# Optimization experiments

Measured on AMD Instinct MI355X. Metric: run time of the kernel, lower is better.

Reference implementation:

```python
import jax, jax.numpy as jnp
import numpy as np

VOCAB, EMB, QLEN, DLEN, K = 100000, 300, 256, 8192, 5


def prelu(x, a):
    return jnp.where(x >= 0, x, a * x)


def apply_conv(x, filt, a):
    # x: (L, E), filt: (E, 1, fs, E) -- matches torch F.conv2d(OIHW)
    fs = filt.shape[2]
    pad = fs // 2 + 1
    inp = x[None, None, :, :]  # (1,1,L,E)
    out = jax.lax.conv_general_dilated(
        inp, filt, window_strides=(1, 1), padding=[(pad, pad), (0, 0)],
        dimension_numbers=('NCHW', 'OIHW', 'NCHW'))  # (1,E,L',1)
    out = prelu(out, a)
    out = out[:, :, -x.shape[0]:, 0]          # keep last L rows -> (1,E,L)
    out = jnp.transpose(out, (0, 2, 1))[0]    # (L,E)
    return out + x


def cosine_sim(A, B):
    # (Q,E) x (D,E) -> (Q,D)
    num = A @ B.T
    den = jnp.linalg.norm(A, axis=1)[:, None] * jnp.linalg.norm(B, axis=1)[None, :]
    return num / den


def pool(sim):
    # sort-based k-max pooling == top_k (same set of values)
    top = jax.lax.top_k(sim, K)[0]           # (Q,K) descending
    avg = top.sum(-1) / float(K)
    mx = top[..., 0]
    return jnp.stack([mx, avg], axis=-1)      # (Q,2)


def score(pooled_list, w1, b1, w2, b2, a1, a2):
    x = jnp.concatenate(pooled_list, axis=-1)  # (Q,8)
    lo = prelu(x @ w1.T + b1, a1)              # dropout is identity in eval
    lo = prelu(lo @ w2.T + b2, a2)[..., 0]     # (Q,)
    return lo.sum(-1) / lo.shape[-1]


def setup_inputs() -> dict:
    key = jax.random.key(0)
    ks = jax.random.split(key, 12)
    doc1 = jax.random.randint(ks[0], (DLEN,), 0, VOCAB)
    doc2 = jax.random.randint(ks[1], (DLEN,), 0, VOCAB)
    question = jax.random.randint(ks[2], (QLEN,), 0, VOCAB)
    doc1_sim = jax.random.uniform(ks[3], (DLEN, QLEN), dtype=jnp.float32)
    doc2_sim = jax.random.uniform(ks[4], (DLEN, QLEN), dtype=jnp.float32)
    embeds = jax.random.normal(ks[5], (VOCAB, EMB), dtype=jnp.float32)
    filt_bi = jax.random.normal(ks[6], (EMB, 1, 2, EMB), dtype=jnp.float32)
    filt_tri = jax.random.normal(ks[7], (EMB, 1, 3, EMB), dtype=jnp.float32)
    w1 = jax.random.normal(ks[8], (8, 8), dtype=jnp.float32) * 0.3
    b1 = jnp.zeros((8,), jnp.float32)
    w2 = jax.random.normal(ks[9], (1, 8), dtype=jnp.float32) * 0.3
    b2 = jnp.zeros((1,), jnp.float32)
    a_bi = jnp.float32(0.25); a_tri = jnp.float32(0.25)
    a1 = jnp.float32(0.25); a2 = jnp.float32(0.25)
    return dict(doc1=doc1, doc2=doc2, question=question, doc1_sim=doc1_sim,
                doc2_sim=doc2_sim, embeds=embeds, filt_bi=filt_bi,
                filt_tri=filt_tri, a_bi=a_bi, a_tri=a_tri, w1=w1, b1=b1,
                w2=w2, b2=b2, a1=a1, a2=a2)


def reference(doc1, doc2, question, doc1_sim, doc2_sim, embeds, filt_bi,
              filt_tri, a_bi, a_tri, w1, b1, w2, b2, a1, a2):
    sim_oh1 = doc1_sim.T  # (Q,D)
    sim_oh2 = doc2_sim.T
    qe = embeds[question]
    d1e = embeds[doc1]
    d2e = embeds[doc2]
    qmask = (question > 1).astype(jnp.float32)
    m1 = qmask[:, None] * (doc1 > 1).astype(jnp.float32)[None, :]
    m2 = qmask[:, None] * (doc2 > 1).astype(jnp.float32)[None, :]
    ins1 = cosine_sim(qe, d1e) * m1
    ins2 = cosine_sim(qe, d2e) * m2
    q_bi = apply_conv(qe, filt_bi, a_bi)
    q_tri = apply_conv(qe, filt_tri, a_tri)
    d1_bi = apply_conv(d1e, filt_bi, a_bi)
    d1_tri = apply_conv(d1e, filt_tri, a_tri)
    d2_bi = apply_conv(d2e, filt_bi, a_bi)
    d2_tri = apply_conv(d2e, filt_tri, a_tri)
    s1_bi = cosine_sim(q_bi, d1_bi)
    s2_bi = cosine_sim(q_bi, d2_bi)
    s1_tri = cosine_sim(q_tri, d1_tri)
    s2_tri = cosine_sim(q_tri, d2_tri)
    d1_emit = score([pool(sim_oh1), pool(ins1), pool(s1_bi), pool(s1_tri)],
                    w1, b1, w2, b2, a1, a2)
    d2_emit = score([pool(sim_oh2), pool(ins2), pool(s2_bi), pool(s2_tri)],
                    w1, b1, w2, b2, a1, a2)
    # MarginRankingLoss(margin=0.9), y=1, batch of 1
    loss1 = jnp.maximum(0.0, -(d1_emit - d2_emit) + 0.9)
    loss2 = loss1 * 0.0
    return (loss1, d1_emit, d2_emit, loss1, loss2)
```

## Files before the change

### kernel.cpp

```cpp
#include <hip/hip_runtime.h>

#define EMB   300
#define QLEN  256
#define DLEN  8192
#define KTOP  5
#define STR   320
#define STRB  640

typedef __attribute__((ext_vector_type(8))) short short8v;
typedef __attribute__((ext_vector_type(4))) float f32x4;

__device__ inline float bf2f(short u) {
    return __uint_as_float(((unsigned int)(unsigned short)u) << 16);
}
__device__ inline short f2bf(float f) {
    unsigned int x = __float_as_uint(f);
    unsigned int r = x + 0x7fffu + ((x >> 16) & 1u);
    return (short)(r >> 16);
}
__device__ inline void gload_lds16(const void* g, void* l) {
    __builtin_amdgcn_global_load_lds((const __attribute__((address_space(1))) void*)g,
                                     (__attribute__((address_space(3))) void*)l, 16, 0, 0);
}
__device__ inline int swz128(int a) { return a ^ (((a >> 7) & 7) << 4); }

#define INSERT5(arr, v)                                                          \
    if ((v) > arr[4]) {                                                          \
        arr[4] = (v);                                                            \
        if (arr[4] > arr[3]) { float t_ = arr[4]; arr[4] = arr[3]; arr[3] = t_; }\
        if (arr[3] > arr[2]) { float t_ = arr[3]; arr[3] = arr[2]; arr[2] = t_; }\
        if (arr[2] > arr[1]) { float t_ = arr[2]; arr[2] = arr[1]; arr[1] = t_; }\
        if (arr[1] > arr[0]) { float t_ = arr[1]; arr[1] = arr[0]; arr[0] = t_; }\
    }

struct PrepArgs {
    const float* embeds;
    const int* toks[3]; short* out[3]; float* ssq[3]; int rows[3];
    const float* filt[2]; short* fout[2];
    float* convssq;
};

__global__ void prep(PrepArgs pa) {
    if (blockIdx.x >= 4646) {
        int idx = (blockIdx.x - 4646) * 256 + threadIdx.x;
        if (idx < 8320) {
            float4 z = {0.f, 0.f, 0.f, 0.f};
            *(float4*)(pa.convssq + idx * 4) = z;
        }
        return;
    }
    int W = blockIdx.x * 4 + (threadIdx.x >> 6);
    int lane = threadIdx.x & 63;
    int e0 = lane * 8;
    if (W < 16664) {
        int s, r;
        if (W < 264) { s = 0; r = W; }
        else if (W < 8464) { s = 1; r = W - 264; }
        else { s = 2; r = W - 8464; }
        int rows = pa.rows[s];
        short8v ov = {0, 0, 0, 0, 0, 0, 0, 0};
        float sum = 0.f;
        if (r < rows && e0 < 300) {
            const float* src = pa.embeds + (long)pa.toks[s][r] * EMB;
            float4 f0 = *(const float4*)(src + e0);
            ov[0] = f2bf(f0.x); ov[1] = f2bf(f0.y); ov[2] = f2bf(f0.z); ov[3] = f2bf(f0.w);
            sum = f0.x * f0.x + f0.y * f0.y + f0.z * f0.z + f0.w * f0.w;
            if (e0 < 296) {
                float4 f1 = *(const float4*)(src + e0 + 4);
                ov[4] = f2bf(f1.x); ov[5] = f2bf(f1.y); ov[6] = f2bf(f1.z); ov[7] = f2bf(f1.w);
                sum += f1.x * f1.x + f1.y * f1.y + f1.z * f1.z + f1.w * f1.w;
            }
        }
        if (e0 < STR) *(short8v*)(pa.out[s] + (long)r * STR + e0) = ov;
        #pragma unroll
        for (int off = 32; off > 0; off >>= 1) sum += __shfl_down(sum, off, 64);
        if (lane == 0 && r < rows) pa.ssq[s][r] = sum;
    } else {
        int w2 = W - 16664;
        int s = (w2 < 768) ? 0 : 1;
        int R = (s == 0) ? w2 : w2 - 768;
        int o = (s == 0) ? (R >> 1) : (R / 3);
        short8v ov = {0, 0, 0, 0, 0, 0, 0, 0};
        if (o < EMB && e0 < 300) {
            const float* src = pa.filt[s] + (long)R * EMB;
            float4 f0 = *(const float4*)(src + e0);
            ov[0] = f2bf(f0.x); ov[1] = f2bf(f0.y); ov[2] = f2bf(f0.z); ov[3] = f2bf(f0.w);
            if (e0 < 296) {
                float4 f1 = *(const float4*)(src + e0 + 4);
                ov[4] = f2bf(f1.x); ov[5] = f2bf(f1.y); ov[6] = f2bf(f1.z); ov[7] = f2bf(f1.w);
            }
        }
        if (e0 < STR) *(short8v*)(pa.fout[s] + (long)R * STR + e0) = ov;
    }
}

#define GEMM_PRELUDE64                                                        \
    int tid = threadIdx.x, lane = tid & 63, w = tid >> 6;                     \
    int wr = w >> 1, wc = w & 1;                                              \
    int arow[2], acol[2], brow[4], bcol[4];                                   \
    _Pragma("unroll")                                                         \
    for (int i_ = 0; i_ < 2; ++i_) {                                          \
        int lg_ = swz128(w * 2048 + i_ * 1024 + lane * 16);                   \
        arow[i_] = lg_ >> 7; acol[i_] = lg_ & 127;                            \
    }                                                                         \
    _Pragma("unroll")                                                         \
    for (int i_ = 0; i_ < 4; ++i_) {                                          \
        int lg_ = swz128(w * 4096 + i_ * 1024 + lane * 16);                   \
        brow[i_] = lg_ >> 7; bcol[i_] = lg_ & 127;                            \
    }

#define STAGE64(t) do { int kb_ = (t) * 128;                                  \
    _Pragma("unroll")                                                         \
    for (int i_ = 0; i_ < 2; ++i_)                                            \
        gload_lds16(Ab + (size_t)arow[i_] * STRB + kb_ + acol[i_],            \
                    AsB + w * 2048 + i_ * 1024);                              \
    _Pragma("unroll")                                                         \
    for (int i_ = 0; i_ < 4; ++i_)                                            \
        gload_lds16(Bb + (size_t)brow[i_] * ldbB + kb_ + bcol[i_],            \
                    BsB + w * 4096 + i_ * 1024);                              \
    } while (0)

#define COMPUTE64 do {                                                        \
    _Pragma("unroll")                                                         \
    for (int h_ = 0; h_ < 2; ++h_) {                                          \
        short8v a_[2], b_[4];                                                 \
        _Pragma("unroll")                                                     \
        for (int f_ = 0; f_ < 2; ++f_) {                                      \
            int la_ = (wr * 32 + f_ * 16 + (lane & 15)) * 128                 \
                      + ((lane >> 4) << 4) + h_ * 64;                         \
            a_[f_] = *(const short8v*)(AsB + swz128(la_));                    \
        }                                                                     \
        _Pragma("unroll")                                                     \
        for (int f_ = 0; f_ < 4; ++f_) {                                      \
            int lb_ = (wc * 64 + f_ * 16 + (lane & 15)) * 128                 \
                      + ((lane >> 4) << 4) + h_ * 64;                         \
            b_[f_] = *(const short8v*)(BsB + swz128(lb_));                    \
        }                                                                     \
        _Pragma("unroll")                                                     \
        for (int mf_ = 0; mf_ < 2; ++mf_)                                     \
            _Pragma("unroll")                                                 \
            for (int nf_ = 0; nf_ < 4; ++nf_)                                 \
                acc[mf_][nf_] = __builtin_amdgcn_mfma_f32_16x16x32_bf16(      \
                    a_[mf_], b_[nf_], acc[mf_][nf_], 0, 0, 0);                \
    } } while (0)

#define GEMM_MAIN64(nt) do {                                                  \
    for (int t_ = 0; t_ < (nt); ++t_) {                                       \
        if (t_ > 0) __syncthreads();                                          \
        STAGE64(t_);                                                          \
        __syncthreads();                                                      \
        COMPUTE64;                                                            \
    } } while (0)

__device__ inline void topk_reduce_store(float top[KTOP], float (*buf)[KTOP], int t,
                                         float* feat, int q, int c0) {
    #pragma unroll
    for (int i = 0; i < KTOP; ++i) buf[t][i] = top[i];
    __syncthreads();
    for (int stride = 128; stride >= 1; stride >>= 1) {
        if (t < stride) {
            float arr[KTOP];
            #pragma unroll
            for (int i = 0; i < KTOP; ++i) arr[i] = buf[t][i];
            #pragma unroll
            for (int r = 0; r < KTOP; ++r) { float v = buf[t + stride][r]; INSERT5(arr, v); }
            #pragma unroll
            for (int i = 0; i < KTOP; ++i) buf[t][i] = arr[i];
        }
        __syncthreads();
    }
    if (t == 0) {
        float mx = buf[0][0];
        float sum = buf[0][0] + buf[0][1] + buf[0][2] + buf[0][3] + buf[0][4];
        feat[(long)q * 8 + c0] = mx;
        feat[(long)q * 8 + c0 + 1] = sum / (float)KTOP;
    }
}

struct ConvSlice { const short* A; const short* F; short* O; float* ssq;
                   const float* alpha; int fs; int shift; };
struct ConvOhArgs { ConvSlice s[6]; const float* S1; const float* S2; float* part; };

__global__ __launch_bounds__(256) void conv_oh(ConvOhArgs args) {
    int orig = blockIdx.x;
    if (orig >= 1560) {
        int r2 = orig - 1560;
        int doc = r2 >> 7, dblk = r2 & 127;
        const float* S = doc == 0 ? args.S1 : args.S2;
        int t = threadIdx.x;
        const float* base = S + (size_t)dblk * 64 * QLEN + t;
        float top[KTOP];
        #pragma unroll
        for (int i = 0; i < KTOP; ++i) top[i] = -3.4e38f;
        float vb[16];
        #pragma unroll
        for (int g = 0; g < 4; ++g) {
            #pragma unroll
            for (int j = 0; j < 16; ++j)
                vb[j] = base[(size_t)(g * 16 + j) * QLEN];
            #pragma unroll
            for (int j = 0; j < 16; ++j) INSERT5(top, vb[j]);
        }
        float* dst = args.part + ((size_t)((6 + doc) * 128 + dblk) * QLEN + t) * KTOP;
        #pragma unroll
        for (int i = 0; i < KTOP; ++i) dst[i] = top[i];
        return;
    }
    int lin = orig;
    int o = (lin & 7) * 195 + (lin >> 3);
    int z;
    if (o < 384) { z = 3; }
    else if (o < 768) { z = 5; o -= 384; }
    else if (o < 780) { z = 1; o -= 768; }
    else if (o < 1164) { z = 2; o -= 780; }
    else if (o < 1548) { z = 4; o -= 1164; }
    else { z = 0; o -= 1548; }
    ConvSlice sl;
    switch (z) {
        case 0: sl = args.s[0]; break; case 1: sl = args.s[1]; break;
        case 2: sl = args.s[2]; break; case 3: sl = args.s[3]; break;
        case 4: sl = args.s[4]; break; default: sl = args.s[5]; break;
    }
    int x = o % 3, y = o / 3;
    int m0 = y * 64, n0 = x * 128;
    int ldbB = sl.fs * STRB;

    __shared__ char smem[24576];
    char* AsB = smem;
    char* BsB = smem + 8192;
    GEMM_PRELUDE64
    const char* Ab = (const char*)sl.A + (size_t)(m0 + sl.shift) * STRB;
    const char* Bb = (const char*)sl.F + (size_t)n0 * ldbB;
    int nt = sl.fs * 5;
    float al = *sl.alpha;

    f32x4 acc[2][4] = {};
    GEMM_MAIN64(nt);

    #pragma unroll
    for (int mf = 0; mf < 2; ++mf) {
        #pragma unroll
        for (int j = 0; j < 4; ++j) {
            int r = m0 + wr * 32 + mf * 16 + (lane >> 4) * 4 + j;
            float p = 0.f;
            #pragma unroll
            for (int nf = 0; nf < 4; ++nf) {
                int c = n0 + wc * 64 + nf * 16 + (lane & 15);
                short ov = 0;
                if (c < EMB) {
                    float v = acc[mf][nf][j];
                    v = v >= 0.f ? v : al * v;
                    v += bf2f(sl.A[(size_t)r * STR + c]);
                    ov = f2bf(v);
                    p += v * v;
                }
                if (c < STR) sl.O[(size_t)r * STR + c] = ov;
            }
            p += __shfl_xor(p, 1, 64);
            p += __shfl_xor(p, 2, 64);
            p += __shfl_xor(p, 4, 64);
            p += __shfl_xor(p, 8, 64);
            if ((lane & 15) == 0) atomicAdd(sl.ssq + r, p);
        }
    }
}

struct SimSlice { const short* D; const short* Q; const float* dssq; const float* qssq;
                  const int* dtok; int mask; };
struct SimArgs { SimSlice s[6]; const int* qtok; float* part; };

__global__ __launch_bounds__(256) void sim_mfma(SimArgs args) {
    int lin = blockIdx.x;
    int wk = (lin & 7) * 192 + (lin >> 3);
    int s = wk >> 8; int rem = wk & 255; int x = rem & 1; int dblk = rem >> 1;
    SimSlice sl;
    switch (s) {
        case 0: sl = args.s[0]; break; case 1: sl = args.s[1]; break;
        case 2: sl = args.s[2]; break; case 3: sl = args.s[3]; break;
        case 4: sl = args.s[4]; break; default: sl = args.s[5]; break;
    }
    int m0 = dblk * 64, n0 = x * 128;
    const int ldbB = STRB;

    __shared__ char AsB[8192];
    __shared__ char BsB[16384];
    GEMM_PRELUDE64
    const char* Ab = (const char*)sl.D + (size_t)m0 * STRB;
    const char* Bb = (const char*)sl.Q + (size_t)n0 * STRB;

    f32x4 acc[2][4] = {};
    GEMM_MAIN64(5);

    float dinvv[2][4];
    int dtokv[2][4];
    #pragma unroll
    for (int mf = 0; mf < 2; ++mf) {
        int r0 = m0 + wr * 32 + mf * 16 + (lane >> 4) * 4;
        float4 dv = *(const float4*)(sl.dssq + r0);
        dinvv[mf][0] = rsqrtf(dv.x); dinvv[mf][1] = rsqrtf(dv.y);
        dinvv[mf][2] = rsqrtf(dv.z); dinvv[mf][3] = rsqrtf(dv.w);
        if (sl.mask) {
            int4 tv = *(const int4*)(sl.dtok + r0);
            dtokv[mf][0] = tv.x; dtokv[mf][1] = tv.y; dtokv[mf][2] = tv.z; dtokv[mf][3] = tv.w;
        }
    }
    __syncthreads();
    float (*lds5)[128][KTOP] = (float (*)[128][KTOP])AsB;

    #pragma unroll
    for (int nf = 0; nf < 4; ++nf) {
        int c = n0 + wc * 64 + nf * 16 + (lane & 15);
        float qs = rsqrtf(sl.qssq[c]);
        bool qok = sl.mask ? (args.qtok[c] > 1) : true;
        float top[KTOP];
        #pragma unroll
        for (int i = 0; i < KTOP; ++i) top[i] = -3.4e38f;
        #pragma unroll
        for (int mf = 0; mf < 2; ++mf)
            #pragma unroll
            for (int j = 0; j < 4; ++j) {
                float v = acc[mf][nf][j] * qs * dinvv[mf][j];
                if (sl.mask && (!qok || dtokv[mf][j] <= 1)) v = 0.f;
                INSERT5(top, v);
            }
        #pragma unroll
        for (int st = 16; st <= 32; st <<= 1) {
            float o[KTOP];
            #pragma unroll
            for (int i = 0; i < KTOP; ++i) o[i] = __shfl_xor(top[i], st, 64);
            #pragma unroll
            for (int i = 0; i < KTOP; ++i) { float v = o[i]; INSERT5(top, v); }
        }
        if (lane < 16) {
            int ql = wc * 64 + nf * 16 + lane;
            #pragma unroll
            for (int i = 0; i < KTOP; ++i) lds5[wr][ql][i] = top[i];
        }
    }
    __syncthreads();
    if (tid < 128) {
        float arr[KTOP];
        #pragma unroll
        for (int i = 0; i < KTOP; ++i) arr[i] = lds5[0][tid][i];
        #pragma unroll
        for (int i = 0; i < KTOP; ++i) { float v = lds5[1][tid][i]; INSERT5(arr, v); }
        int q = n0 + tid;
        float* dst = args.part + ((size_t)(s * 128 + dblk) * QLEN + q) * KTOP;
        #pragma unroll
        for (int i = 0; i < KTOP; ++i) dst[i] = arr[i];
    }
}

__global__ void pool_reduce(const float* __restrict__ part,
                            float* __restrict__ feat1, float* __restrict__ feat2) {
    int s = blockIdx.y, q = blockIdx.x, t = threadIdx.x;
    __shared__ float buf[256][KTOP];
    float top[KTOP];
    #pragma unroll
    for (int i = 0; i < KTOP; ++i) top[i] = -3.4e38f;
    if (t < 128) {
        const float* src = part + ((size_t)(s * 128 + t) * QLEN + q) * KTOP;
        #pragma unroll
        for (int i = 0; i < KTOP; ++i) { float v = src[i]; INSERT5(top, v); }
    }
    float* feat = (s < 6) ? (s < 3 ? feat1 : feat2) : (s == 6 ? feat1 : feat2);
    int c0 = (s < 6) ? 2 + 2 * (s % 3) : 0;
    topk_reduce_store(top, buf, t, feat, q, c0);
}

__global__ void final_score(const float* __restrict__ feat1, const float* __restrict__ feat2,
                            const float* __restrict__ w1, const float* __restrict__ b1,
                            const float* __restrict__ w2, const float* __restrict__ b2,
                            const float* __restrict__ a1p, const float* __restrict__ a2p,
                            float* __restrict__ out) {
    __shared__ float s1buf[256], s2buf[256];
    int q = threadIdx.x;
    float a1 = *a1p, a2 = *a2p;
    float v[2];
    #pragma unroll
    for (int dsel = 0; dsel < 2; ++dsel) {
        const float* feat = dsel == 0 ? feat1 : feat2;
        float x[8];
        #pragma unroll
        for (int i = 0; i < 8; ++i) x[i] = feat[q * 8 + i];
        float lo[8];
        #pragma unroll
        for (int j = 0; j < 8; ++j) {
            float s = b1[j];
            #pragma unroll
            for (int i = 0; i < 8; ++i) s += x[i] * w1[j * 8 + i];
            lo[j] = s >= 0.f ? s : a1 * s;
        }
        float s2v = b2[0];
        #pragma unroll
        for (int j = 0; j < 8; ++j) s2v += lo[j] * w2[j];
        v[dsel] = s2v >= 0.f ? s2v : a2 * s2v;
    }
    s1buf[q] = v[0];
    s2buf[q] = v[1];
    __syncthreads();
    for (int st = 128; st >= 1; st >>= 1) {
        if (q < st) { s1buf[q] += s1buf[q + st]; s2buf[q] += s2buf[q + st]; }
        __syncthreads();
    }
    if (q == 0) {
        float d1 = s1buf[0] / (float)QLEN;
        float d2 = s2buf[0] / (float)QLEN;
        float loss1 = fmaxf(0.f, -(d1 - d2) + 0.9f);
        out[0] = loss1; out[1] = d1; out[2] = d2; out[3] = loss1; out[4] = 0.f;
    }
}

extern "C" void kernel_launch(void* const* d_in, const int* in_sizes, int n_in,
                              void* d_out, int out_size, void* d_ws, size_t ws_size,
                              hipStream_t stream) {
    const int*   doc1     = (const int*)d_in[0];
    const int*   doc2     = (const int*)d_in[1];
    const int*   question = (const int*)d_in[2];
    const float* doc1_sim = (const float*)d_in[3];
    const float* doc2_sim = (const float*)d_in[4];
    const float* embeds   = (const float*)d_in[5];
    const float* filt_bi  = (const float*)d_in[6];
    const float* filt_tri = (const float*)d_in[7];
    const float* a_bi     = (const float*)d_in[8];
    const float* a_tri    = (const float*)d_in[9];
    const float* w1       = (const float*)d_in[10];
    const float* b1       = (const float*)d_in[11];
    const float* w2       = (const float*)d_in[12];
    const float* b2       = (const float*)d_in[13];
    const float* a1       = (const float*)d_in[14];
    const float* a2       = (const float*)d_in[15];
    float* out = (float*)d_out;

    float* ws = (float*)d_ws;
    size_t off = 0;
    auto allocf = [&](size_t n) { float* p = ws + off; off += n; return p; };
    float* feat1 = allocf(QLEN * 8);
    float* feat2 = allocf(QLEN * 8);
    float* ssq_qe  = allocf(QLEN);
    float* ssq_d1e = allocf(DLEN);
    float* ssq_d2e = allocf(DLEN);
    float* convssq = allocf(2 * QLEN + 4 * DLEN);
    float* ssq_qbi  = convssq;
    float* ssq_qtri = convssq + QLEN;
    float* ssq_d1bi  = convssq + 2 * QLEN;
    float* ssq_d1tri = convssq + 2 * QLEN + DLEN;
    float* ssq_d2bi  = convssq + 2 * QLEN + 2 * DLEN;
    float* ssq_d2tri = convssq + 2 * QLEN + 3 * DLEN;
    float* part = allocf((size_t)8 * 128 * QLEN * KTOP);
    off = (off + 7) & ~(size_t)7;

    short* hb = (short*)(ws + off);
    size_t hoff = 0;
    auto alloch = [&](size_t n) { short* p = hb + hoff; hoff += n; return p; };
    const size_t QH = (size_t)(QLEN + 8) * STR;
    const size_t DH = (size_t)(DLEN + 8) * STR;
    short* qe_h   = alloch(QH);
    short* qbi_h  = alloch(QH);
    short* qtri_h = alloch(QH);
    short* d1e_h   = alloch(DH);
    short* d1bi_h  = alloch(DH);
    short* d1tri_h = alloch(DH);
    short* d2e_h   = alloch(DH);
    short* d2bi_h  = alloch(DH);
    short* d2tri_h = alloch(DH);
    short* fbi_h  = alloch((size_t)384 * 2 * STR);
    short* ftri_h = alloch((size_t)384 * 3 * STR);

    PrepArgs pa;
    pa.embeds = embeds;
    pa.toks[0] = question; pa.out[0] = qe_h;  pa.ssq[0] = ssq_qe;  pa.rows[0] = QLEN;
    pa.toks[1] = doc1;     pa.out[1] = d1e_h; pa.ssq[1] = ssq_d1e; pa.rows[1] = DLEN;
    pa.toks[2] = doc2;     pa.out[2] = d2e_h; pa.ssq[2] = ssq_d2e; pa.rows[2] = DLEN;
    pa.filt[0] = filt_bi;  pa.fout[0] = fbi_h;
    pa.filt[1] = filt_tri; pa.fout[1] = ftri_h;
    pa.convssq = convssq;
    prep<<<dim3(4679), 256, 0, stream>>>(pa);

    ConvOhArgs ca;
    ca.s[0] = { qe_h,  fbi_h,  qbi_h,  ssq_qbi,  a_bi,  2, 1 };
    ca.s[1] = { qe_h,  ftri_h, qtri_h, ssq_qtri, a_tri, 3, 0 };
    ca.s[2] = { d1e_h, fbi_h,  d1bi_h, ssq_d1bi, a_bi,  2, 1 };
    ca.s[3] = { d1e_h, ftri_h, d1tri_h,ssq_d1tri,a_tri, 3, 0 };
    ca.s[4] = { d2e_h, fbi_h,  d2bi_h, ssq_d2bi, a_bi,  2, 1 };
    ca.s[5] = { d2e_h, ftri_h, d2tri_h,ssq_d2tri,a_tri, 3, 0 };
    ca.S1 = doc1_sim; ca.S2 = doc2_sim;
    ca.part = part;
    conv_oh<<<dim3(1816), 256, 0, stream>>>(ca);

    SimArgs sa;
    sa.s[0] = { d1e_h,   qe_h,   ssq_d1e,   ssq_qe,   doc1, 1 };
    sa.s[1] = { d1bi_h,  qbi_h,  ssq_d1bi,  ssq_qbi,  doc1, 0 };
    sa.s[2] = { d1tri_h, qtri_h, ssq_d1tri, ssq_qtri, doc1, 0 };
    sa.s[3] = { d2e_h,   qe_h,   ssq_d2e,   ssq_qe,   doc2, 1 };
    sa.s[4] = { d2bi_h,  qbi_h,  ssq_d2bi,  ssq_qbi,  doc2, 0 };
    sa.s[5] = { d2tri_h, qtri_h, ssq_d2tri, ssq_qtri, doc2, 0 };
    sa.qtok = question;
    sa.part = part;
    sim_mfma<<<dim3(1536), 256, 0, stream>>>(sa);

    pool_reduce<<<dim3(QLEN, 8), 256, 0, stream>>>(part, feat1, feat2);

    final_score<<<dim3(1), 256, 0, stream>>>(feat1, feat2, w1, b1, w2, b2, a1, a2, out);
}
```

Measured before the change: 105.9 us.

## Halve GEMM K-tile to 64 and fuse pool reduce with final score via last-block counter

```diff
diff --git a/kernel.cpp b/kernel.cpp
--- a/kernel.cpp
+++ b/kernel.cpp
@@ -22,7 +22,7 @@
     __builtin_amdgcn_global_load_lds((const __attribute__((address_space(1))) void*)g,
                                      (__attribute__((address_space(3))) void*)l, 16, 0, 0);
 }
-__device__ inline int swz128(int a) { return a ^ (((a >> 7) & 7) << 4); }
+__device__ inline int swz64(int a) { return a ^ (((a >> 7) & 7) << 4); }
 
 #define INSERT5(arr, v)                                                          \
     if ((v) > arr[4]) {                                                          \
@@ -43,7 +43,7 @@
 __global__ void prep(PrepArgs pa) {
     if (blockIdx.x >= 4646) {
         int idx = (blockIdx.x - 4646) * 256 + threadIdx.x;
-        if (idx < 8320) {
+        if (idx < 8321) {
             float4 z = {0.f, 0.f, 0.f, 0.f};
             *(float4*)(pa.convssq + idx * 4) = z;
         }
@@ -94,62 +94,51 @@
     }
 }
 
-#define GEMM_PRELUDE64                                                        \
+#define GEMM_PRELUDE32                                                        \
     int tid = threadIdx.x, lane = tid & 63, w = tid >> 6;                     \
     int wr = w >> 1, wc = w & 1;                                              \
-    int arow[2], acol[2], brow[4], bcol[4];                                   \
+    int arow0, acol0, brow[2], bcol[2];                                       \
+    { int lg_ = swz64(w * 1024 + lane * 16);                                  \
+      arow0 = lg_ >> 6; acol0 = lg_ & 63; }                                   \
     _Pragma("unroll")                                                         \
     for (int i_ = 0; i_ < 2; ++i_) {                                          \
-        int lg_ = swz128(w * 2048 + i_ * 1024 + lane * 16);                   \
-        arow[i_] = lg_ >> 7; acol[i_] = lg_ & 127;                            \
+        int lg_ = swz64(w * 2048 + i_ * 1024 + lane * 16);                    \
+        brow[i_] = lg_ >> 6; bcol[i_] = lg_ & 63;                             \
+    }
+
+#define STAGE32(t) do { int kb_ = (t) * 64;                                   \
+    gload_lds16(Ab + (size_t)arow0 * STRB + kb_ + acol0, AsB + w * 1024);     \
+    gload_lds16(Bb + (size_t)brow[0] * ldbB + kb_ + bcol[0], BsB + w * 2048); \
+    gload_lds16(Bb + (size_t)brow[1] * ldbB + kb_ + bcol[1],                  \
+                BsB + w * 2048 + 1024);                                       \
+    } while (0)
+
+#define COMPUTE32 do {                                                        \
+    short8v a_[2], b_[4];                                                     \
+    _Pragma("unroll")                                                         \
+    for (int f_ = 0; f_ < 2; ++f_) {                                          \
+        int la_ = (wr * 32 + f_ * 16 + (lane & 15)) * 64 + ((lane >> 4) << 4);\
+        a_[f_] = *(const short8v*)(AsB + swz64(la_));                         \
     }                                                                         \
     _Pragma("unroll")                                                         \
-    for (int i_ = 0; i_ < 4; ++i_) {                                          \
-        int lg_ = swz128(w * 4096 + i_ * 1024 + lane * 16);                   \
-        brow[i_] = lg_ >> 7; bcol[i_] = lg_ & 127;                            \
-    }
-
-#define STAGE64(t) do { int kb_ = (t) * 128;                                  \
+    for (int f_ = 0; f_ < 4; ++f_) {                                          \
+        int lb_ = (wc * 64 + f_ * 16 + (lane & 15)) * 64 + ((lane >> 4) << 4);\
+        b_[f_] = *(const short8v*)(BsB + swz64(lb_));                         \
+    }                                                                         \
     _Pragma("unroll")                                                         \
-    for (int i_ = 0; i_ < 2; ++i_)                                            \
-        gload_lds16(Ab + (size_t)arow[i_] * STRB + kb_ + acol[i_],            \
-                    AsB + w * 2048 + i_ * 1024);                              \
-    _Pragma("unroll")                                                         \
-    for (int i_ = 0; i_ < 4; ++i_)                                            \
-        gload_lds16(Bb + (size_t)brow[i_] * ldbB + kb_ + bcol[i_],            \
-                    BsB + w * 4096 + i_ * 1024);                              \
+    for (int mf_ = 0; mf_ < 2; ++mf_)                                         \
+        _Pragma("unroll")                                                     \
+        for (int nf_ = 0; nf_ < 4; ++nf_)                                     \
+            acc[mf_][nf_] = __builtin_amdgcn_mfma_f32_16x16x32_bf16(          \
+                a_[mf_], b_[nf_], acc[mf_][nf_], 0, 0, 0);                    \
     } while (0)
 
-#define COMPUTE64 do {                                                        \
-    _Pragma("unroll")                                                         \
-    for (int h_ = 0; h_ < 2; ++h_) {                                          \
-        short8v a_[2], b_[4];                                                 \
-        _Pragma("unroll")                                                     \
-        for (int f_ = 0; f_ < 2; ++f_) {                                      \
-            int la_ = (wr * 32 + f_ * 16 + (lane & 15)) * 128                 \
-                      + ((lane >> 4) << 4) + h_ * 64;                         \
-            a_[f_] = *(const short8v*)(AsB + swz128(la_));                    \
-        }                                                                     \
-        _Pragma("unroll")                                                     \
-        for (int f_ = 0; f_ < 4; ++f_) {                                      \
-            int lb_ = (wc * 64 + f_ * 16 + (lane & 15)) * 128                 \
-                      + ((lane >> 4) << 4) + h_ * 64;                         \
-            b_[f_] = *(const short8v*)(BsB + swz128(lb_));                    \
-        }                                                                     \
-        _Pragma("unroll")                                                     \
-        for (int mf_ = 0; mf_ < 2; ++mf_)                                     \
-            _Pragma("unroll")                                                 \
-            for (int nf_ = 0; nf_ < 4; ++nf_)                                 \
-                acc[mf_][nf_] = __builtin_amdgcn_mfma_f32_16x16x32_bf16(      \
-                    a_[mf_], b_[nf_], acc[mf_][nf_], 0, 0, 0);                \
-    } } while (0)
-
-#define GEMM_MAIN64(nt) do {                                                  \
+#define GEMM_MAIN32(nt) do {                                                  \
     for (int t_ = 0; t_ < (nt); ++t_) {                                       \
         if (t_ > 0) __syncthreads();                                          \
-        STAGE64(t_);                                                          \
+        STAGE32(t_);                                                          \
         __syncthreads();                                                      \
-        COMPUTE64;                                                            \
+        COMPUTE32;                                                            \
     } } while (0)
 
 __device__ inline void topk_reduce_store(float top[KTOP], float (*buf)[KTOP], int t,
@@ -225,17 +214,17 @@
     int m0 = y * 64, n0 = x * 128;
     int ldbB = sl.fs * STRB;
 
-    __shared__ char smem[24576];
+    __shared__ char smem[12288];
     char* AsB = smem;
-    char* BsB = smem + 8192;
-    GEMM_PRELUDE64
+    char* BsB = smem + 4096;
+    GEMM_PRELUDE32
     const char* Ab = (const char*)sl.A + (size_t)(m0 + sl.shift) * STRB;
     const char* Bb = (const char*)sl.F + (size_t)n0 * ldbB;
-    int nt = sl.fs * 5;
+    int nt = sl.fs * 10;
     float al = *sl.alpha;
 
     f32x4 acc[2][4] = {};
-    GEMM_MAIN64(nt);
+    GEMM_MAIN32(nt);
 
     #pragma unroll
     for (int mf = 0; mf < 2; ++mf) {
@@ -282,14 +271,15 @@
     int m0 = dblk * 64, n0 = x * 128;
     const int ldbB = STRB;
 
-    __shared__ char AsB[8192];
-    __shared__ char BsB[16384];
-    GEMM_PRELUDE64
+    __shared__ char smem[12288];
+    char* AsB = smem;
+    char* BsB = smem + 4096;
+    GEMM_PRELUDE32
     const char* Ab = (const char*)sl.D + (size_t)m0 * STRB;
     const char* Bb = (const char*)sl.Q + (size_t)n0 * STRB;
 
     f32x4 acc[2][4] = {};
-    GEMM_MAIN64(5);
+    GEMM_MAIN32(10);
 
     float dinvv[2][4];
     int dtokv[2][4];
@@ -305,7 +295,7 @@
         }
     }
     __syncthreads();
-    float (*lds5)[128][KTOP] = (float (*)[128][KTOP])AsB;
+    float (*lds5)[128][KTOP] = (float (*)[128][KTOP])smem;
 
     #pragma unroll
     for (int nf = 0; nf < 4; ++nf) {
@@ -351,63 +341,70 @@
     }
 }
 
-__global__ void pool_reduce(const float* __restrict__ part,
-                            float* __restrict__ feat1, float* __restrict__ feat2) {
-    int s = blockIdx.y, q = blockIdx.x, t = threadIdx.x;
+struct RFArgs {
+    const float* part; float* feat1; float* feat2;
+    unsigned int* counter;
+    const float* w1; const float* b1; const float* w2; const float* b2;
+    const float* a1; const float* a2; float* out;
+};
+
+__global__ void reduce_final(RFArgs ra) {
+    int s = blockIdx.x >> 8, q = blockIdx.x & 255, t = threadIdx.x;
     __shared__ float buf[256][KTOP];
-    float top[KTOP];
-    #pragma unroll
-    for (int i = 0; i < KTOP; ++i) top[i] = -3.4e38f;
-    if (t < 128) {
-        const float* src = part + ((size_t)(s * 128 + t) * QLEN + q) * KTOP;
-        #pragma unroll
-        for (int i = 0; i < KTOP; ++i) { float v = src[i]; INSERT5(top, v); }
-    }
-    float* feat = (s < 6) ? (s < 3 ? feat1 : feat2) : (s == 6 ? feat1 : feat2);
-    int c0 = (s < 6) ? 2 + 2 * (s % 3) : 0;
-    topk_reduce_store(top, buf, t, feat, q, c0);
-}
-
-__global__ void final_score(const float* __restrict__ feat1, const float* __restrict__ feat2,
-                            const float* __restrict__ w1, const float* __restrict__ b1,
-                            const float* __restrict__ w2, const float* __restrict__ b2,
-                            const float* __restrict__ a1p, const float* __restrict__ a2p,
-                            float* __restrict__ out) {
+    {
+        float top[KTOP];
+        #pragma unroll
+        for (int i = 0; i < KTOP; ++i) top[i] = -3.4e38f;
+        if (t < 128) {
+            const float* src = ra.part + ((size_t)(s * 128 + t) * QLEN + q) * KTOP;
+            #pragma unroll
+            for (int i = 0; i < KTOP; ++i) { float v = src[i]; INSERT5(top, v); }
+        }
+        float* feat = (s < 6) ? (s < 3 ? ra.feat1 : ra.feat2) : (s == 6 ? ra.feat1 : ra.feat2);
+        int c0 = (s < 6) ? 2 + 2 * (s % 3) : 0;
+        topk_reduce_store(top, buf, t, feat, q, c0);
+    }
+    __threadfence();
+    __shared__ int is_last;
+    if (t == 0) is_last = (atomicAdd(ra.counter, 1u) == 2047u) ? 1 : 0;
+    __syncthreads();
+    if (!is_last) return;
+    __threadfence();
+
     __shared__ float s1buf[256], s2buf[256];
-    int q = threadIdx.x;
-    float a1 = *a1p, a2 = *a2p;
+    float a1 = *ra.a1, a2 = *ra.a2;
     float v[2];
     #pragma unroll
     for (int dsel = 0; dsel < 2; ++dsel) {
-        const float* feat = dsel == 0 ? feat1 : feat2;
+        const float* feat = dsel == 0 ? ra.feat1 : ra.feat2;
         float x[8];
         #pragma unroll
-        for (int i = 0; i < 8; ++i) x[i] = feat[q * 8 + i];
+        for (int i = 0; i < 8; ++i) x[i] = feat[t * 8 + i];
         float lo[8];
         #pragma unroll
         for (int j = 0; j < 8; ++j) {
-            float s = b1[j];
-            #pragma unroll
-            for (int i = 0; i < 8; ++i) s += x[i] * w1[j * 8 + i];
-            lo[j] = s >= 0.f ? s : a1 * s;
-        }
-        float s2v = b2[0];
-        #pragma unroll
-        for (int j = 0; j < 8; ++j) s2v += lo[j] * w2[j];
+            float sacc = ra.b1[j];
+            #pragma unroll
+            for (int i = 0; i < 8; ++i) sacc += x[i] * ra.w1[j * 8 + i];
+            lo[j] = sacc >= 0.f ? sacc : a1 * sacc;
+        }
+        float s2v = ra.b2[0];
+        #pragma unroll
+        for (int j = 0; j < 8; ++j) s2v += lo[j] * ra.w2[j];
         v[dsel] = s2v >= 0.f ? s2v : a2 * s2v;
     }
-    s1buf[q] = v[0];
-    s2buf[q] = v[1];
+    s1buf[t] = v[0];
+    s2buf[t] = v[1];
     __syncthreads();
     for (int st = 128; st >= 1; st >>= 1) {
-        if (q < st) { s1buf[q] += s1buf[q + st]; s2buf[q] += s2buf[q + st]; }
+        if (t < st) { s1buf[t] += s1buf[t + st]; s2buf[t] += s2buf[t + st]; }
         __syncthreads();
     }
-    if (q == 0) {
+    if (t == 0) {
         float d1 = s1buf[0] / (float)QLEN;
         float d2 = s2buf[0] / (float)QLEN;
         float loss1 = fmaxf(0.f, -(d1 - d2) + 0.9f);
-        out[0] = loss1; out[1] = d1; out[2] = d2; out[3] = loss1; out[4] = 0.f;
+        ra.out[0] = loss1; ra.out[1] = d1; ra.out[2] = d2; ra.out[3] = loss1; ra.out[4] = 0.f;
     }
 }
 
@@ -440,13 +437,14 @@
     float* ssq_qe  = allocf(QLEN);
     float* ssq_d1e = allocf(DLEN);
     float* ssq_d2e = allocf(DLEN);
-    float* convssq = allocf(2 * QLEN + 4 * DLEN);
+    float* convssq = allocf(2 * QLEN + 4 * DLEN + 4);
     float* ssq_qbi  = convssq;
     float* ssq_qtri = convssq + QLEN;
     float* ssq_d1bi  = convssq + 2 * QLEN;
     float* ssq_d1tri = convssq + 2 * QLEN + DLEN;
     float* ssq_d2bi  = convssq + 2 * QLEN + 2 * DLEN;
     float* ssq_d2tri = convssq + 2 * QLEN + 3 * DLEN;
+    unsigned int* counter = (unsigned int*)(convssq + 2 * QLEN + 4 * DLEN);
     float* part = allocf((size_t)8 * 128 * QLEN * KTOP);
     off = (off + 7) & ~(size_t)7;
 
@@ -499,7 +497,8 @@
     sa.part = part;
     sim_mfma<<<dim3(1536), 256, 0, stream>>>(sa);
 
-    pool_reduce<<<dim3(QLEN, 8), 256, 0, stream>>>(part, feat1, feat2);
-
-    final_score<<<dim3(1), 256, 0, stream>>>(feat1, feat2, w1, b1, w2, b2, a1, a2, out);
-}
+    RFArgs ra;
+    ra.part = part; ra.feat1 = feat1; ra.feat2 = feat2; ra.counter = counter;
+    ra.w1 = w1; ra.b1 = b1; ra.w2 = w2; ra.b2 = b2; ra.a1 = a1; ra.a2 = a2; ra.out = out;
+    reduce_final<<<dim3(2048), 256, 0, stream>>>(ra);
+}
```

New measurement: 297.4 us. 2.81x slower.

## Use per-wave private LDS staging in conv GEMM to drop block barriers

Applied to the files above, without the earlier changes.

```diff
diff --git a/kernel.cpp b/kernel.cpp
--- a/kernel.cpp
+++ b/kernel.cpp
@@ -152,6 +152,66 @@
         COMPUTE64;                                                            \
     } } while (0)
 
+#define GEMM_PRELUDE_WP                                                       \
+    int tid = threadIdx.x, lane = tid & 63, w = tid >> 6;                     \
+    int wr = w >> 1, wc = w & 1;                                              \
+    int abase = w * 4096;                                                     \
+    int bbase = 16384 + w * 8192;                                             \
+    int grow8[8], gcol8[8];                                                   \
+    _Pragma("unroll")                                                         \
+    for (int i_ = 0; i_ < 8; ++i_) {                                          \
+        int lg_ = swz128(i_ * 1024 + lane * 16);                              \
+        grow8[i_] = lg_ >> 7; gcol8[i_] = lg_ & 127;                          \
+    }
+
+#define STAGE_WP(t) do { int kb_ = (t) * 128;                                 \
+    _Pragma("unroll")                                                         \
+    for (int i_ = 0; i_ < 4; ++i_)                                            \
+        gload_lds16(AbW + (size_t)grow8[i_] * STRB + kb_ + gcol8[i_],         \
+                    smem + abase + i_ * 1024);                                \
+    _Pragma("unroll")                                                         \
+    for (int i_ = 0; i_ < 8; ++i_)                                            \
+        gload_lds16(BbW + (size_t)grow8[i_] * ldbB + kb_ + gcol8[i_],         \
+                    smem + bbase + i_ * 1024);                                \
+    } while (0)
+
+#define COMPUTE_WP do {                                                       \
+    _Pragma("unroll")                                                         \
+    for (int h_ = 0; h_ < 2; ++h_) {                                          \
+        short8v a_[2], b_[4];                                                 \
+        _Pragma("unroll")                                                     \
+        for (int f_ = 0; f_ < 2; ++f_) {                                      \
+            int la_ = abase + (f_ * 16 + (lane & 15)) * 128                   \
+                      + ((lane >> 4) << 4) + h_ * 64;                         \
+            a_[f_] = *(const short8v*)(smem + swz128(la_));                   \
+        }                                                                     \
+        _Pragma("unroll")                                                     \
+        for (int f_ = 0; f_ < 4; ++f_) {                                      \
+            int lb_ = bbase + (f_ * 16 + (lane & 15)) * 128                   \
+                      + ((lane >> 4) << 4) + h_ * 64;                         \
+            b_[f_] = *(const short8v*)(smem + swz128(lb_));                   \
+        }                                                                     \
+        _Pragma("unroll")                                                     \
+        for (int mf_ = 0; mf_ < 2; ++mf_)                                     \
+            _Pragma("unroll")                                                 \
+            for (int nf_ = 0; nf_ < 4; ++nf_)                                 \
+                acc[mf_][nf_] = __builtin_amdgcn_mfma_f32_16x16x32_bf16(      \
+                    a_[mf_], b_[nf_], acc[mf_][nf_], 0, 0, 0);                \
+    } } while (0)
+
+#define GEMM_MAIN_WP(nt) do {                                                 \
+    for (int t_ = 0; t_ < (nt); ++t_) {                                       \
+        if (t_ > 0) {                                                         \
+            asm volatile("s_waitcnt lgkmcnt(0)" ::: "memory");                \
+            __builtin_amdgcn_sched_barrier(0);                                \
+        }                                                                     \
+        STAGE_WP(t_);                                                         \
+        asm volatile("s_waitcnt vmcnt(0)" ::: "memory");                      \
+        __builtin_amdgcn_sched_barrier(0);                                    \
+        COMPUTE_WP;                                                           \
+        __builtin_amdgcn_sched_barrier(0);                                    \
+    } } while (0)
+
 __device__ inline void topk_reduce_store(float top[KTOP], float (*buf)[KTOP], int t,
                                          float* feat, int q, int c0) {
     #pragma unroll
@@ -182,6 +242,7 @@
 struct ConvOhArgs { ConvSlice s[6]; const float* S1; const float* S2; float* part; };
 
 __global__ __launch_bounds__(256) void conv_oh(ConvOhArgs args) {
+    __shared__ char smem[49152];
     int orig = blockIdx.x;
     if (orig >= 1560) {
         int r2 = orig - 1560;
@@ -225,17 +286,14 @@
     int m0 = y * 64, n0 = x * 128;
     int ldbB = sl.fs * STRB;
 
-    __shared__ char smem[24576];
-    char* AsB = smem;
-    char* BsB = smem + 8192;
-    GEMM_PRELUDE64
-    const char* Ab = (const char*)sl.A + (size_t)(m0 + sl.shift) * STRB;
-    const char* Bb = (const char*)sl.F + (size_t)n0 * ldbB;
+    GEMM_PRELUDE_WP
+    const char* AbW = (const char*)sl.A + (size_t)(m0 + wr * 32 + sl.shift) * STRB;
+    const char* BbW = (const char*)sl.F + (size_t)(n0 + wc * 64) * ldbB;
     int nt = sl.fs * 5;
     float al = *sl.alpha;
 
     f32x4 acc[2][4] = {};
-    GEMM_MAIN64(nt);
+    GEMM_MAIN_WP(nt);
 
     #pragma unroll
     for (int mf = 0; mf < 2; ++mf) {
```

Result: slower. 127.1 us (+19.9%).
